# Optimization experiments

Hardware: AMD Instinct MI355X
Metric: run time of the kernel (lower is better)

The kernel has to match this reference:

```python
import jax, jax.numpy as jnp
import numpy as np
from jax import lax

UNITS = 500

def _lstm_scan(x, h0, c0, Wk, Wr, b):
    # x: [B,T,D]; precompute input projection for all timesteps.
    xz = jnp.einsum('btd,dk->btk', x, Wk) + b  # [B,T,4U]
    def step(carry, xz_t):
        h, c = carry
        z = xz_t + h @ Wr  # [B,4U]
        i, f, g, o = jnp.split(z, 4, axis=-1)  # Keras gate order: i,f,c,o
        i = jax.nn.sigmoid(i)
        f = jax.nn.sigmoid(f)
        g = jnp.tanh(g)
        o = jax.nn.sigmoid(o)
        c = f * c + i * g
        h = o * jnp.tanh(c)
        return (h, c), h
    (hT, cT), hs = lax.scan(step, (h0, c0), jnp.swapaxes(xz, 0, 1))  # hs: [T,B,U]
    return jnp.swapaxes(hs, 0, 1), hT, cT


def setup_inputs() -> dict:
    key = jax.random.key(0)
    ks = jax.random.split(key, 8)
    B, T, D, U = 64, 256, 512, UNITS
    sk = 1.0 / np.sqrt(D)
    sr = 1.0 / np.sqrt(U)
    return {
        'x': jax.random.normal(ks[0], (B, T, D), jnp.float32),
        'h_f': jnp.zeros((B, U), jnp.float32),
        'c_f': jnp.zeros((B, U), jnp.float32),
        'h_b': jnp.zeros((B, U), jnp.float32),
        'c_b': jnp.zeros((B, U), jnp.float32),
        'Wk_f': jax.random.normal(ks[1], (D, 4 * U), jnp.float32) * sk,
        'Wr_f': jax.random.normal(ks[2], (U, 4 * U), jnp.float32) * sr,
        'b_f': jnp.zeros((4 * U,), jnp.float32),
        'Wk_b': jax.random.normal(ks[3], (D, 4 * U), jnp.float32) * sk,
        'Wr_b': jax.random.normal(ks[4], (U, 4 * U), jnp.float32) * sr,
        'b_b': jnp.zeros((4 * U,), jnp.float32),
    }


def reference(x, h_f, c_f, h_b, c_b, Wk_f, Wr_f, b_f, Wk_b, Wr_b, b_b):
    # Forward-direction LSTM over t = 0..T-1
    y_f, _, _ = _lstm_scan(x, h_f, c_f, Wk_f, Wr_f, b_f)
    # Backward-direction LSTM: process reversed sequence, then reverse outputs
    # back to time order (Keras Bidirectional with return_sequences=True).
    y_b_rev, _, _ = _lstm_scan(x[:, ::-1], h_b, c_b, Wk_b, Wr_b, b_b)
    y_b = y_b_rev[:, ::-1]
    return jnp.concatenate([y_f, y_b], axis=-1)  # merge='concat' -> [B,T,2U]
```

## Files before the change

### kernel.cpp

```cpp
#include <hip/hip_runtime.h>
#include <hip/hip_fp16.h>
#include <cstdint>
#include <cstddef>

#define B_    64
#define T_    256
#define D_    512
#define U_    500
#define UP_   512
#define NCOL_ 2048
#define K_    1024

typedef _Float16 f16x8 __attribute__((ext_vector_type(8)));
typedef float    f32x4 __attribute__((ext_vector_type(4)));

#define OFF_X   0ull
#define OFF_W   16777216ull
#define OFF_B   25165824ull
#define OFF_H   25182208ull

#define LXA 0
#define LXB 16384
#define LZP 32768
#define LDS_BYTES 53248

#define TAGMASK 0x0003000300030003ull

#define GLD_LDS16(g, l) \
  __builtin_amdgcn_global_load_lds((const __attribute__((address_space(1))) void*)(g), \
                                   (__attribute__((address_space(3))) void*)(l), 16, 0, 0)


__global__ void prep_x(const float* __restrict__ x, _Float16* __restrict__ xf) {
  size_t base = ((size_t)blockIdx.x * 256 + threadIdx.x) * 8;
  const float4* p = (const float4*)(x + base);
  float4 a = p[0], b = p[1];
  f16x8 v;
  v[0] = (_Float16)a.x; v[1] = (_Float16)a.y; v[2] = (_Float16)a.z; v[3] = (_Float16)a.w;
  v[4] = (_Float16)b.x; v[5] = (_Float16)b.y; v[6] = (_Float16)b.z; v[7] = (_Float16)b.w;
  *(f16x8*)(xf + base) = v;
}

__global__ void prep_w(const float* __restrict__ Wkf, const float* __restrict__ Wrf,
                       const float* __restrict__ Wkb, const float* __restrict__ Wrb,
                       const float* __restrict__ bf,  const float* __restrict__ bb,
                       _Float16* __restrict__ Wc, float* __restrict__ bcomb) {
  size_t gid = (size_t)blockIdx.x * 256 + threadIdx.x;
  int dir = (int)(gid >> 18);
  int rem = (int)(gid & 262143);
  int col = rem >> 7;
  int k0  = (rem & 127) << 3;
  const float* Wk = dir ? Wkb : Wkf;
  const float* Wr = dir ? Wrb : Wrf;
  int g = (col >> 4) & 3, du = col & 15, utc = col >> 6;
  int ug = utc * 16 + du;
  bool valid = (ug < U_);
  int c4 = g * U_ + ug;
  f16x8 out;
#pragma unroll
  for (int kk = 0; kk < 8; ++kk) {
    int k = k0 + kk;
    float v = 0.f;
    if (valid) {
      if (k < D_) v = Wk[(size_t)k * (4 * U_) + c4];
      else { int u = k - D_; if (u < U_) v = Wr[(size_t)u * (4 * U_) + c4]; }
    }
    out[kk] = (_Float16)v;
  }
  *(f16x8*)(Wc + ((size_t)dir * NCOL_ + col) * K_ + k0) = out;

  if (gid < 4096) {
    int d2 = (int)(gid >> 11), c2 = (int)(gid & 2047);
    int g2 = (c2 >> 4) & 3, du2 = c2 & 15, ut2 = c2 >> 6;
    int ug2 = ut2 * 16 + du2;
    const float* bs = d2 ? bb : bf;
    bcomb[gid] = (ug2 < U_) ? bs[g2 * U_ + ug2] : 0.f;
  }
}

__global__ void prep_hb(const float* __restrict__ hf, const float* __restrict__ hb,
                        _Float16* __restrict__ hbuf) {
  int idx = blockIdx.x * 256 + threadIdx.x;
  int dir = idx >> 15;
  int rem = idx & 32767;
  int bt = rem >> 13, r = (rem >> 9) & 15, u = rem & 511;
  const float* h0 = dir ? hb : hf;
  float v = (u < U_) ? h0[(size_t)(bt * 16 + r) * U_ + u] : 0.f;
  int gi = dir * 4 + bt;
  union { _Float16 f; unsigned short s; } cv;
  cv.f = (_Float16)v;
  cv.s &= 0xFFFC;
  ((unsigned short*)hbuf)[(size_t)(gi * 2 + 0) * 8192 + (u >> 4) * 256 + r * 16 + (u & 15)] = cv.s;
}

__global__ __launch_bounds__(256, 1) void lstm_scan(
    const _Float16* __restrict__ xf, const _Float16* __restrict__ Wc,
    const float* __restrict__ bc, const float* __restrict__ cf,
    const float* __restrict__ cb, _Float16* __restrict__ hbuf,
    float* __restrict__ y)
{
  __shared__ __align__(16) char lds[LDS_BYTES];
  const int tid  = threadIdx.x;
  const int lane = tid & 63;
  const int w    = tid >> 6;
  const int bid  = blockIdx.x;
  const int grp  = bid & 7;
  const int dir  = grp >> 2;
  const int bt   = grp & 3;
  const int ut   = bid >> 3;

  const int c15  = lane & 15;
  const int kg   = lane >> 4;
  const int arow = c15;

  f16x8 breg[4][8];
  {
    const _Float16* wbase = Wc + ((size_t)dir * NCOL_ + (size_t)ut * 64) * K_ + w * 256;
#pragma unroll
    for (int ct = 0; ct < 4; ++ct)
#pragma unroll
      for (int ks = 0; ks < 8; ++ks)
        breg[ct][ks] = *(const f16x8*)(wbase + (size_t)(ct * 16 + c15) * K_ + ks * 32 + kg * 8);
  }

  const int r0 = tid >> 4, du0 = tid & 15;
  const int ug0 = ut * 16 + du0;
  float bg[4];
#pragma unroll
  for (int g = 0; g < 4; ++g) bg[g] = bc[dir * NCOL_ + ut * 64 + g * 16 + du0];
  const float* cin = dir ? cb : cf;
  float c = (ug0 < U_) ? cin[(size_t)(bt * 16 + r0) * U_ + ug0] : 0.f;

  const int gi = dir * 4 + bt;
  _Float16* hb = hbuf + (size_t)gi * 2 * 8192;

#pragma unroll
  for (int tt = 0; tt < 2; ++tt) {
    const int t_x0 = dir ? (T_ - 1 - tt) : tt;
    char* dst = lds + (tt ? LXB : LXA);
    for (int rr = 0; rr < 4; ++rr) {
      int r = w * 4 + rr;
      const char* src = (const char*)(xf + ((size_t)(bt * 16 + r) * T_ + t_x0) * D_)
                        + ((lane ^ (r & 7)) << 4);
      GLD_LDS16(src, dst + r * 1024);
    }
  }
  __syncthreads();

  float* zpw = (float*)(lds + LZP) + w * 1280;
  const float* zr = (const float*)(lds + LZP);

  for (int t = 0; t < T_; ++t) {
    const int t_x = dir ? (T_ - 1 - t) : t;

    f32x4 acc[4] = {{0.f,0.f,0.f,0.f},{0.f,0.f,0.f,0.f},{0.f,0.f,0.f,0.f},{0.f,0.f,0.f,0.f}};

    if (w >= 2) {
      const unsigned long long* hr =
          (const unsigned long long*)(hb + (size_t)(t & 1) * 8192);
      unsigned tag = (unsigned)(t & 255);
      unsigned long long expect =
          (unsigned long long)(tag & 3)
        | ((unsigned long long)((tag >> 2) & 3) << 16)
        | ((unsigned long long)((tag >> 4) & 3) << 32)
        | ((unsigned long long)((tag >> 6) & 3) << 48);
      const int chb = (w - 2) * 32;

      unsigned long long v[16];
      while (true) {
#pragma unroll
        for (int ks = 0; ks < 8; ++ks) {
          int ch = chb + ks * 4 + kg;
          int bidx = (ch >> 1) * 64 + arow * 4 + (ch & 1) * 2;
          v[2*ks]   = __hip_atomic_load(hr + bidx,     __ATOMIC_RELAXED, __HIP_MEMORY_SCOPE_AGENT);
          v[2*ks+1] = __hip_atomic_load(hr + bidx + 1, __ATOMIC_RELAXED, __HIP_MEMORY_SCOPE_AGENT);
        }
        bool ok = true;
#pragma unroll
        for (int i = 0; i < 16; ++i) ok &= ((v[i] & TAGMASK) == expect);
        if (__all(ok)) break;
        __builtin_amdgcn_s_sleep(1);
      }
#pragma unroll
      for (int ks = 0; ks < 8; ++ks) {
        union { unsigned long long u[2]; f16x8 f; } tmp;
        tmp.u[0] = v[2*ks]; tmp.u[1] = v[2*ks+1];
#pragma unroll
        for (int ct = 0; ct < 4; ++ct)
          acc[ct] = __builtin_amdgcn_mfma_f32_16x16x32_f16(tmp.f, breg[ct][ks], acc[ct], 0, 0, 0);
      }
    } else {
      const char* xb = lds + ((t & 1) ? LXB : LXA);
#pragma unroll
      for (int ks = 0; ks < 8; ++ks) {
        int ch = w * 32 + ks * 4 + kg;
        f16x8 a = *(const f16x8*)(xb + arow * 1024 + ((ch ^ (arow & 7)) << 4));
#pragma unroll
        for (int ct = 0; ct < 4; ++ct)
          acc[ct] = __builtin_amdgcn_mfma_f32_16x16x32_f16(a, breg[ct][ks], acc[ct], 0, 0, 0);
      }
    }

#pragma unroll
    for (int ct = 0; ct < 4; ++ct)
      *(f32x4*)(zpw + (ct * 16 + c15) * 20 + kg * 4) = acc[ct];
    __syncthreads();

    if (t + 2 < T_) {
      const int t_n = dir ? (T_ - 3 - t) : (t + 2);
      char* dst = lds + ((t & 1) ? LXB : LXA);
      for (int rr = 0; rr < 4; ++rr) {
        int r = w * 4 + rr;
        const char* src = (const char*)(xf + ((size_t)(bt * 16 + r) * T_ + t_n) * D_)
                          + ((lane ^ (r & 7)) << 4);
        GLD_LDS16(src, dst + r * 1024);
      }
    }

    float h;
    {
      float z[4];
#pragma unroll
      for (int g = 0; g < 4; ++g) {
        int cb2 = (g * 16 + du0) * 20 + r0;
        z[g] = bg[g] + zr[cb2] + zr[1280 + cb2] + zr[2560 + cb2] + zr[3840 + cb2];
      }
      float ig = 1.f / (1.f + __expf(-z[0]));
      float fg = 1.f / (1.f + __expf(-z[1]));
      float e2 = __expf(2.f * z[2]);
      float gg = (e2 - 1.f) / (e2 + 1.f);
      float og = 1.f / (1.f + __expf(-z[3]));
      c = fg * c + ig * gg;
      float ec = __expf(2.f * c);
      float th = (ec - 1.f) / (ec + 1.f);
      h = og * th;
    }

    {
      unsigned ptag = (unsigned)((t + 1) & 255);
      union { _Float16 f; unsigned short s; } cv;
      cv.f = (_Float16)h;
      unsigned tagged = ((unsigned)cv.s & 0xFFFCu) | ((ptag >> (2 * (du0 & 3))) & 3u);
      unsigned pair = tagged | ((unsigned)__shfl_xor((int)tagged, 1, 64) << 16);
      unsigned other = (unsigned)__shfl_xor((int)pair, 2, 64);
      if ((du0 & 3) == 0) {
        unsigned long long u = (unsigned long long)pair | ((unsigned long long)other << 32);
        unsigned long long* hbw = (unsigned long long*)(hb + (size_t)((t + 1) & 1) * 8192);
        __hip_atomic_store(hbw + ut * 64 + r0 * 4 + (du0 >> 2), u,
                           __ATOMIC_RELAXED, __HIP_MEMORY_SCOPE_AGENT);
      }
    }

    if (ug0 < U_)
      y[((size_t)(bt * 16 + r0) * T_ + t_x) * (2 * U_) + dir * U_ + ug0] = h;

    __syncthreads();
  }
}

extern "C" void kernel_launch(void* const* d_in, const int* in_sizes, int n_in,
                              void* d_out, int out_size, void* d_ws, size_t ws_size,
                              hipStream_t stream) {
  (void)in_sizes; (void)n_in; (void)out_size; (void)ws_size;
  const float* x    = (const float*)d_in[0];
  const float* h_f  = (const float*)d_in[1];
  const float* c_f  = (const float*)d_in[2];
  const float* h_b  = (const float*)d_in[3];
  const float* c_b  = (const float*)d_in[4];
  const float* Wk_f = (const float*)d_in[5];
  const float* Wr_f = (const float*)d_in[6];
  const float* b_f  = (const float*)d_in[7];
  const float* Wk_b = (const float*)d_in[8];
  const float* Wr_b = (const float*)d_in[9];
  const float* b_b  = (const float*)d_in[10];

  char* ws = (char*)d_ws;
  _Float16* xf    = (_Float16*)(ws + OFF_X);
  _Float16* Wc    = (_Float16*)(ws + OFF_W);
  float*    bcomb = (float*)   (ws + OFF_B);
  _Float16* hbuf  = (_Float16*)(ws + OFF_H);
  float*    y     = (float*)d_out;

  prep_x<<<4096, 256, 0, stream>>>(x, xf);
  prep_w<<<2048, 256, 0, stream>>>(Wk_f, Wr_f, Wk_b, Wr_b, b_f, b_b, Wc, bcomb);
  prep_hb<<<256, 256, 0, stream>>>(h_f, h_b, hbuf);

  lstm_scan<<<256, 256, 0, stream>>>(xf, Wc, bcomb, c_f, c_b, hbuf, y);
}
```

Baseline: 483.8 us.

## Split both input and recurrent K across all waves and drop one barrier per step

Previously two waves did the input-projection MFMAs and two did the recurrent-h MFMAs for each timestep. Now every wave does a quarter of both. The recurrent h loads are issued first, the x-part MFMAs run while they are in flight, and only 4 recurrent k-steps per wave remain after the h tags arrive. This shortens the serial critical path of each step. The gate pre-activation scratch in LDS is double-buffered by timestep parity, so the trailing __syncthreads is replaced by a single lgkmcnt wait and s_barrier per step. Shared memory becomes dynamic (73728 bytes, set via hipFuncSetAttribute). The async x prefetch into LDS now has less barrier protection, which risks a race.

```diff
diff --git a/kernel.cpp b/kernel.cpp
--- a/kernel.cpp
+++ b/kernel.cpp
@@ -19,10 +19,11 @@
 #define OFF_B   25165824ull
 #define OFF_H   25182208ull
 
-#define LXA 0
-#define LXB 16384
-#define LZP 32768
-#define LDS_BYTES 53248
+#define LXA  0
+#define LXB  16384
+#define LZP0 32768
+#define LZP1 53248
+#define LDS_BYTES 73728
 
 #define TAGMASK 0x0003000300030003ull
 
@@ -99,7 +100,7 @@
     const float* __restrict__ cb, _Float16* __restrict__ hbuf,
     float* __restrict__ y)
 {
-  __shared__ __align__(16) char lds[LDS_BYTES];
+  extern __shared__ __align__(16) char lds[];
   const int tid  = threadIdx.x;
   const int lane = tid & 63;
   const int w    = tid >> 6;
@@ -113,14 +114,17 @@
   const int kg   = lane >> 4;
   const int arow = c15;
 
-  f16x8 breg[4][8];
+  f16x8 bx[4][4], bh[4][4];
   {
-    const _Float16* wbase = Wc + ((size_t)dir * NCOL_ + (size_t)ut * 64) * K_ + w * 256;
+    const _Float16* wbase = Wc + ((size_t)dir * NCOL_ + (size_t)ut * 64) * K_;
 #pragma unroll
     for (int ct = 0; ct < 4; ++ct)
 #pragma unroll
-      for (int ks = 0; ks < 8; ++ks)
-        breg[ct][ks] = *(const f16x8*)(wbase + (size_t)(ct * 16 + c15) * K_ + ks * 32 + kg * 8);
+      for (int ks = 0; ks < 4; ++ks) {
+        const _Float16* cl = wbase + (size_t)(ct * 16 + c15) * K_ + w * 128 + ks * 32 + kg * 8;
+        bx[ct][ks] = *(const f16x8*)cl;
+        bh[ct][ks] = *(const f16x8*)(cl + 512);
+      }
   }
 
   const int r0 = tid >> 4, du0 = tid & 15;
@@ -147,64 +151,72 @@
   }
   __syncthreads();
 
-  float* zpw = (float*)(lds + LZP) + w * 1280;
-  const float* zr = (const float*)(lds + LZP);
-
+#pragma unroll 1
   for (int t = 0; t < T_; ++t) {
     const int t_x = dir ? (T_ - 1 - t) : t;
 
+    const unsigned long long* hr =
+        (const unsigned long long*)(hb + (size_t)(t & 1) * 8192);
+    unsigned long long v[8];
+#pragma unroll
+    for (int ks = 0; ks < 4; ++ks) {
+      int ch = w * 16 + ks * 4 + kg;
+      int bidx = (ch >> 1) * 64 + arow * 4 + (ch & 1) * 2;
+      v[2*ks]   = __hip_atomic_load(hr + bidx,     __ATOMIC_RELAXED, __HIP_MEMORY_SCOPE_AGENT);
+      v[2*ks+1] = __hip_atomic_load(hr + bidx + 1, __ATOMIC_RELAXED, __HIP_MEMORY_SCOPE_AGENT);
+    }
+    __builtin_amdgcn_sched_barrier(0);
+
+    const char* xb = lds + ((t & 1) ? LXB : LXA);
     f32x4 acc[4] = {{0.f,0.f,0.f,0.f},{0.f,0.f,0.f,0.f},{0.f,0.f,0.f,0.f},{0.f,0.f,0.f,0.f}};
-
-    if (w >= 2) {
-      const unsigned long long* hr =
-          (const unsigned long long*)(hb + (size_t)(t & 1) * 8192);
+#pragma unroll
+    for (int ks = 0; ks < 4; ++ks) {
+      int ch = w * 16 + ks * 4 + kg;
+      f16x8 a = *(const f16x8*)(xb + arow * 1024 + ((ch ^ (arow & 7)) << 4));
+#pragma unroll
+      for (int ct = 0; ct < 4; ++ct)
+        acc[ct] = __builtin_amdgcn_mfma_f32_16x16x32_f16(a, bx[ct][ks], acc[ct], 0, 0, 0);
+    }
+
+    {
       unsigned tag = (unsigned)(t & 255);
       unsigned long long expect =
           (unsigned long long)(tag & 3)
         | ((unsigned long long)((tag >> 2) & 3) << 16)
         | ((unsigned long long)((tag >> 4) & 3) << 32)
         | ((unsigned long long)((tag >> 6) & 3) << 48);
-      const int chb = (w - 2) * 32;
-
-      unsigned long long v[16];
       while (true) {
-#pragma unroll
-        for (int ks = 0; ks < 8; ++ks) {
-          int ch = chb + ks * 4 + kg;
+        bool ok = true;
+#pragma unroll
+        for (int i = 0; i < 8; ++i) ok &= ((v[i] & TAGMASK) == expect);
+        if (__all(ok)) break;
+        __builtin_amdgcn_s_sleep(1);
+#pragma unroll
+        for (int ks = 0; ks < 4; ++ks) {
+          int ch = w * 16 + ks * 4 + kg;
           int bidx = (ch >> 1) * 64 + arow * 4 + (ch & 1) * 2;
           v[2*ks]   = __hip_atomic_load(hr + bidx,     __ATOMIC_RELAXED, __HIP_MEMORY_SCOPE_AGENT);
           v[2*ks+1] = __hip_atomic_load(hr + bidx + 1, __ATOMIC_RELAXED, __HIP_MEMORY_SCOPE_AGENT);
         }
-        bool ok = true;
-#pragma unroll
-        for (int i = 0; i < 16; ++i) ok &= ((v[i] & TAGMASK) == expect);
-        if (__all(ok)) break;
-        __builtin_amdgcn_s_sleep(1);
-      }
-#pragma unroll
-      for (int ks = 0; ks < 8; ++ks) {
-        union { unsigned long long u[2]; f16x8 f; } tmp;
-        tmp.u[0] = v[2*ks]; tmp.u[1] = v[2*ks+1];
-#pragma unroll
-        for (int ct = 0; ct < 4; ++ct)
-          acc[ct] = __builtin_amdgcn_mfma_f32_16x16x32_f16(tmp.f, breg[ct][ks], acc[ct], 0, 0, 0);
-      }
-    } else {
-      const char* xb = lds + ((t & 1) ? LXB : LXA);
-#pragma unroll
-      for (int ks = 0; ks < 8; ++ks) {
-        int ch = w * 32 + ks * 4 + kg;
-        f16x8 a = *(const f16x8*)(xb + arow * 1024 + ((ch ^ (arow & 7)) << 4));
-#pragma unroll
-        for (int ct = 0; ct < 4; ++ct)
-          acc[ct] = __builtin_amdgcn_mfma_f32_16x16x32_f16(a, breg[ct][ks], acc[ct], 0, 0, 0);
-      }
-    }
-
+      }
+    }
+
+#pragma unroll
+    for (int ks = 0; ks < 4; ++ks) {
+      union { unsigned long long u[2]; f16x8 f; } tmp;
+      tmp.u[0] = v[2*ks]; tmp.u[1] = v[2*ks+1];
+#pragma unroll
+      for (int ct = 0; ct < 4; ++ct)
+        acc[ct] = __builtin_amdgcn_mfma_f32_16x16x32_f16(tmp.f, bh[ct][ks], acc[ct], 0, 0, 0);
+    }
+
+    float* zpw = (float*)(lds + ((t & 1) ? LZP1 : LZP0)) + w * 1280;
 #pragma unroll
     for (int ct = 0; ct < 4; ++ct)
       *(f32x4*)(zpw + (ct * 16 + c15) * 20 + kg * 4) = acc[ct];
-    __syncthreads();
+
+    asm volatile("s_waitcnt lgkmcnt(0)" ::: "memory");
+    __builtin_amdgcn_s_barrier();
 
     if (t + 2 < T_) {
       const int t_n = dir ? (T_ - 3 - t) : (t + 2);
@@ -219,6 +231,7 @@
 
     float h;
     {
+      const float* zr = (const float*)(lds + ((t & 1) ? LZP1 : LZP0));
       float z[4];
 #pragma unroll
       for (int g = 0; g < 4; ++g) {
@@ -253,8 +266,6 @@
 
     if (ug0 < U_)
       y[((size_t)(bt * 16 + r0) * T_ + t_x) * (2 * U_) + dir * U_ + ug0] = h;
-
-    __syncthreads();
   }
 }
 
@@ -285,5 +296,11 @@
   prep_w<<<2048, 256, 0, stream>>>(Wk_f, Wr_f, Wk_b, Wr_b, b_f, b_b, Wc, bcomb);
   prep_hb<<<256, 256, 0, stream>>>(h_f, h_b, hbuf);
 
-  lstm_scan<<<256, 256, 0, stream>>>(xf, Wc, bcomb, c_f, c_b, hbuf, y);
-}
+  static bool attr_done = false;
+  if (!attr_done) {
+    (void)hipFuncSetAttribute((const void*)lstm_scan,
+                              hipFuncAttributeMaxDynamicSharedMemorySize, LDS_BYTES);
+    attr_done = true;
+  }
+  lstm_scan<<<256, 256, LDS_BYTES, stream>>>(xf, Wc, bcomb, c_f, c_b, hbuf, y);
+}
```

Result: slower. 606.5 us (+25.4%).
